# Kernel optimization log

Hardware: AMD Instinct MI355X
Metric: run time of the kernel (lower is better)

The kernel has to match this reference:

```python
import jax, jax.numpy as jnp
import numpy as np

B, L, C, H = 8, 1024, 512, 8
D = C // H  # head_size = 64


def setup_inputs() -> dict:
    key = jax.random.key(0)
    k1, k2, k3, k4, k5, k6 = jax.random.split(key, 6)
    x = jax.random.normal(k1, (B, L, C), dtype=jnp.float32)
    adj = jax.random.randint(k2, (B, L, L), 0, 2).astype(jnp.float32)
    distance = jax.random.randint(k3, (B, L, L), 0, 3).astype(jnp.float32)
    # nn.Linear(dim, 3*dim, bias=False): stored as y = x @ W; init ~ U(-1/sqrt(C), 1/sqrt(C))
    bound = 1.0 / np.sqrt(C)
    w_qkv = jax.random.uniform(k4, (C, 3 * C), minval=-bound, maxval=bound, dtype=jnp.float32)
    w_proj = jax.random.uniform(k5, (C, C), minval=-bound, maxval=bound, dtype=jnp.float32)
    # struct_gamma is zero-init in the module; use small random values so biases are exercised
    gamma = 0.1 * jax.random.normal(k6, (H, 5), dtype=jnp.float32)
    return {"x": x, "adj": adj, "distance": distance,
            "w_qkv": w_qkv, "w_proj": w_proj, "gamma": gamma}


def reference(x, adj, distance, w_qkv, w_proj, gamma):
    b, l, c = x.shape
    scale = jnp.asarray(np.sqrt(D), x.dtype)
    qkv = x @ w_qkv                                    # [B,L,3C]
    q, k, v = jnp.split(qkv, 3, axis=-1)
    q = q.reshape(b, l, H, D).transpose(0, 2, 1, 3)     # [B,H,L,D]
    k = k.reshape(b, l, H, D).transpose(0, 2, 1, 3)
    v = v.reshape(b, l, H, D).transpose(0, 2, 1, 3)
    s = jnp.einsum('bhid,bhjd->bhij', q, k) / scale     # [B,H,L,L]

    # has_cls=True: zero row 0 and col 0 of adj
    adj_local = adj.at[:, 0, :].set(0.0).at[:, :, 0].set(0.0)
    adj_t = adj_local.transpose(0, 2, 1)
    b_fwd = adj_local                                   # direct edges
    b_bwd = adj_t
    b_dist_fwd = (distance > 0).astype(x.dtype)         # multi-hop reachability
    b_dist_bwd = (distance.transpose(0, 2, 1) > 0).astype(x.dtype)
    b_struct = (jnp.einsum('bik,bjk->bij', adj_local, adj_local) > 0).astype(x.dtype)

    biases = jnp.stack([b_fwd, b_bwd, b_dist_fwd, b_dist_bwd, b_struct], axis=1)  # [B,5,L,L]
    s = s + jnp.einsum('hk,bkij->bhij', gamma, biases)

    attn = jax.nn.softmax(s, axis=-1)
    out = jnp.einsum('bhij,bhjd->bhid', attn, v)        # [B,H,L,D]
    out = out.transpose(0, 2, 1, 3).reshape(b, l, c)
    return out @ w_proj
```

## Files before the change

kernel.cpp:

```cpp
#include <hip/hip_runtime.h>
#include <hip/hip_bf16.h>
#include <stdint.h>

#define NB 8
#define NL 1024
#define NC 512
#define NH 8
#define ND 64

typedef __attribute__((ext_vector_type(8))) short short8;
typedef __attribute__((ext_vector_type(4))) float f32x4;
typedef unsigned long long u64;

__device__ __forceinline__ short f2bf(float f) {
  union { float f; uint32_t u; } v; v.f = f;
  uint32_t r = v.u + 0x7FFFu + ((v.u >> 16) & 1u);
  return (short)(r >> 16);
}

#define MFMA16(a, b, c) __builtin_amdgcn_mfma_f32_16x16x32_bf16((a), (b), (c), 0, 0, 0)

__global__ __launch_bounds__(256) void pack_k(const float* __restrict__ adj,
                                              const float* __restrict__ dist,
                                              u64* __restrict__ padj,
                                              u64* __restrict__ pdist) {
  int row = blockIdx.x;
  int i = row & (NL - 1);
  int wv = threadIdx.x >> 6, lane = threadIdx.x & 63;
  const float* asrc = adj + (size_t)row * NL;
  const float* dsrc = dist + (size_t)row * NL;
  #pragma unroll
  for (int it = 0; it < 4; it++) {
    int j = wv * 256 + it * 64 + lane;
    float a = asrc[j];
    float d = dsrc[j];
    u64 am = __ballot((a != 0.0f) && (i != 0) && (j != 0));
    u64 dm = __ballot(d > 0.0f);
    if (lane == 0) {
      padj[(size_t)row * 16 + wv * 4 + it] = am;
      pdist[(size_t)row * 16 + wv * 4 + it] = dm;
    }
  }
}

__global__ __launch_bounds__(256) void bits_k(const u64* __restrict__ padj,
                                              const u64* __restrict__ pdist,
                                              unsigned char* __restrict__ bits) {
  __shared__ u64 Pi[64][17], Pj[64][17];
  __shared__ u64 DiW[64], DjW[64];
  int b = blockIdx.z, i0 = blockIdx.y * 64, j0 = blockIdx.x * 64;
  int t = threadIdx.x;
  int jw = j0 >> 6, iw = i0 >> 6;
  const u64* pa = padj + (size_t)b * NL * 16;
  const u64* pd = pdist + (size_t)b * NL * 16;
  #pragma unroll
  for (int s = 0; s < 4; s++) {
    int idx = s * 256 + t; int r = idx >> 4, w = idx & 15;
    Pi[r][w] = pa[(size_t)(i0 + r) * 16 + w];
    Pj[r][w] = pa[(size_t)(j0 + r) * 16 + w];
  }
  if (t < 64) DiW[t] = pd[(size_t)(i0 + t) * 16 + jw];
  else if (t < 128) DjW[t - 64] = pd[(size_t)(j0 + t - 64) * 16 + iw];
  __syncthreads();
  const size_t base = (size_t)b * NL * NL;
  int jj0 = (t & 15) * 4;
  #pragma unroll
  for (int s = 0; s < 4; s++) {
    int ii = (t >> 4) + s * 16;
    u64 fwdw = Pi[ii][jw];
    u64 dfw = DiW[ii];
    uint32_t acc = 0;
    #pragma unroll
    for (int q = 0; q < 4; q++) {
      int jj = jj0 + q;
      unsigned v = 0;
      v |= (unsigned)((fwdw >> jj) & 1);
      v |= (unsigned)((Pj[jj][iw] >> ii) & 1) << 1;
      v |= (unsigned)((dfw >> jj) & 1) << 2;
      v |= (unsigned)((DjW[jj] >> ii) & 1) << 3;
      #pragma unroll 1
      for (int w = 0; w < 16; w++) {
        if (Pi[ii][w] & Pj[jj][w]) { v |= 16; break; }
      }
      acc |= v << (8 * q);
    }
    *(uint32_t*)&bits[base + (size_t)(i0 + ii) * NL + j0 + jj0] = acc;
  }
}

__global__ __launch_bounds__(256) void qkv_gemm_k(const float* __restrict__ x,
                                                  const float* __restrict__ w,
                                                  unsigned short* __restrict__ qb,
                                                  unsigned short* __restrict__ kb,
                                                  unsigned short* __restrict__ vb) {
  __shared__ short Al[64][40];
  __shared__ short Bl[64][40];
  int t = threadIdx.x;
  int wv = t >> 6, lane = t & 63, lg = lane >> 4, lm = lane & 15;
  int wr = wv >> 1, wc = wv & 1;
  int M0 = blockIdx.y * 64, N0 = blockIdx.x * 64;
  f32x4 zero4 = {0.f, 0.f, 0.f, 0.f};
  f32x4 acc[2][2] = {{zero4, zero4}, {zero4, zero4}};
  for (int k0 = 0; k0 < NC; k0 += 32) {
    {
      int row = t >> 2, cc = (t & 3) * 8;
      const float* src = x + (size_t)(M0 + row) * NC + k0 + cc;
      float4 v0 = *(const float4*)src;
      float4 v1 = *(const float4*)(src + 4);
      short8 s8;
      s8[0] = f2bf(v0.x); s8[1] = f2bf(v0.y); s8[2] = f2bf(v0.z); s8[3] = f2bf(v0.w);
      s8[4] = f2bf(v1.x); s8[5] = f2bf(v1.y); s8[6] = f2bf(v1.z); s8[7] = f2bf(v1.w);
      *(short8*)&Al[row][cc] = s8;
    }
    {
      int kk = t >> 3, cc = (t & 7) * 8;
      const float* src = w + (size_t)(k0 + kk) * (3 * NC) + N0 + cc;
      float4 v0 = *(const float4*)src;
      float4 v1 = *(const float4*)(src + 4);
      Bl[cc + 0][kk] = f2bf(v0.x); Bl[cc + 1][kk] = f2bf(v0.y);
      Bl[cc + 2][kk] = f2bf(v0.z); Bl[cc + 3][kk] = f2bf(v0.w);
      Bl[cc + 4][kk] = f2bf(v1.x); Bl[cc + 5][kk] = f2bf(v1.y);
      Bl[cc + 6][kk] = f2bf(v1.z); Bl[cc + 7][kk] = f2bf(v1.w);
    }
    __syncthreads();
    short8 af[2], bfr[2];
    af[0] = *(short8*)&Al[wr * 32 + lm][lg * 8];
    af[1] = *(short8*)&Al[wr * 32 + 16 + lm][lg * 8];
    bfr[0] = *(short8*)&Bl[wc * 32 + lm][lg * 8];
    bfr[1] = *(short8*)&Bl[wc * 32 + 16 + lm][lg * 8];
    #pragma unroll
    for (int mi = 0; mi < 2; mi++)
      #pragma unroll
      for (int ni = 0; ni < 2; ni++)
        acc[mi][ni] = MFMA16(af[mi], bfr[ni], acc[mi][ni]);
    __syncthreads();
  }
  #pragma unroll
  for (int mi = 0; mi < 2; mi++)
    #pragma unroll
    for (int ni = 0; ni < 2; ni++)
      #pragma unroll
      for (int r = 0; r < 4; r++) {
        int m = M0 + wr * 32 + mi * 16 + lg * 4 + r;
        int n = N0 + wc * 32 + ni * 16 + lm;
        int which = n >> 9, c = n & 511;
        int h = c >> 6, d = c & 63;
        int bb = m >> 10, ll = m & 1023;
        unsigned short* dst = which == 0 ? qb : (which == 1 ? kb : vb);
        dst[(((size_t)bb * NH + h) * NL + ll) * ND + d] = (unsigned short)f2bf(acc[mi][ni][r]);
      }
}

__global__ __launch_bounds__(256) void attn_k(const unsigned short* __restrict__ qb,
                                              const unsigned short* __restrict__ kb,
                                              const unsigned short* __restrict__ vb,
                                              const unsigned char* __restrict__ bits,
                                              const float* __restrict__ gamma,
                                              unsigned short* __restrict__ ao) {
  __shared__ short Kl[64][72];
  __shared__ short Vt[64][72];
  __shared__ short Pl[64][72];
  __shared__ float lut[32];
  int b = blockIdx.z, h = blockIdx.y, q0 = blockIdx.x * 64;
  int t = threadIdx.x, wv = t >> 6, lane = t & 63, lg = lane >> 4, lm = lane & 15;
  if (t < 32) {
    float s = 0.f;
    #pragma unroll
    for (int k = 0; k < 5; k++) if ((t >> k) & 1) s += gamma[h * 5 + k];
    lut[t] = s;
  }
  const size_t bh = ((size_t)b * NH + h) * NL;
  short8 qf[2];
  {
    const unsigned short* src = qb + (bh + q0 + wv * 16 + lm) * ND + lg * 8;
    qf[0] = *(const short8*)src;
    qf[1] = *(const short8*)(src + 32);
  }
  f32x4 zero4 = {0.f, 0.f, 0.f, 0.f};
  f32x4 oacc[4] = {zero4, zero4, zero4, zero4};
  float m_run[4], l_run[4];
  #pragma unroll
  for (int r = 0; r < 4; r++) { m_run[r] = -1e30f; l_run[r] = 0.f; }
  __syncthreads();
  for (int j0 = 0; j0 < NL; j0 += 64) {
    {
      int r = t >> 2, cc = (t & 3) * 16;
      const unsigned short* ks = kb + (bh + j0 + r) * ND + cc;
      *(short8*)&Kl[r][cc]     = *(const short8*)ks;
      *(short8*)&Kl[r][cc + 8] = *(const short8*)(ks + 8);
      const unsigned short* vs = vb + (bh + j0 + r) * ND + cc;
      short8 v0 = *(const short8*)vs;
      short8 v1 = *(const short8*)(vs + 8);
      #pragma unroll
      for (int jj = 0; jj < 8; jj++) Vt[cc + jj][r] = v0[jj];
      #pragma unroll
      for (int jj = 0; jj < 8; jj++) Vt[cc + 8 + jj][r] = v1[jj];
    }
    __syncthreads();
    f32x4 sf[4];
    #pragma unroll
    for (int ni = 0; ni < 4; ni++) {
      short8 b0 = *(short8*)&Kl[ni * 16 + lm][lg * 8];
      short8 b1 = *(short8*)&Kl[ni * 16 + lm][32 + lg * 8];
      f32x4 c = {0.f, 0.f, 0.f, 0.f};
      c = MFMA16(qf[0], b0, c);
      c = MFMA16(qf[1], b1, c);
      sf[ni] = c;
    }
    float svv[4][4];
    #pragma unroll
    for (int ni = 0; ni < 4; ni++)
      #pragma unroll
      for (int r = 0; r < 4; r++) {
        int qi = q0 + wv * 16 + lg * 4 + r;
        int kj = j0 + ni * 16 + lm;
        unsigned char bt = bits[((size_t)b * NL + qi) * NL + kj];
        svv[ni][r] = sf[ni][r] * 0.125f + lut[bt & 31];
      }
    float nm[4], fac[4], rsum[4];
    #pragma unroll
    for (int r = 0; r < 4; r++) {
      float mx = fmaxf(fmaxf(svv[0][r], svv[1][r]), fmaxf(svv[2][r], svv[3][r]));
      mx = fmaxf(mx, __shfl_xor(mx, 1));
      mx = fmaxf(mx, __shfl_xor(mx, 2));
      mx = fmaxf(mx, __shfl_xor(mx, 4));
      mx = fmaxf(mx, __shfl_xor(mx, 8));
      nm[r] = fmaxf(m_run[r], mx);
      fac[r] = __expf(m_run[r] - nm[r]);
      m_run[r] = nm[r];
      rsum[r] = 0.f;
    }
    #pragma unroll
    for (int ni = 0; ni < 4; ni++)
      #pragma unroll
      for (int r = 0; r < 4; r++) {
        float p = __expf(svv[ni][r] - nm[r]);
        svv[ni][r] = p;
        rsum[r] += p;
      }
    #pragma unroll
    for (int r = 0; r < 4; r++) {
      rsum[r] += __shfl_xor(rsum[r], 1);
      rsum[r] += __shfl_xor(rsum[r], 2);
      rsum[r] += __shfl_xor(rsum[r], 4);
      rsum[r] += __shfl_xor(rsum[r], 8);
      l_run[r] = l_run[r] * fac[r] + rsum[r];
    }
    #pragma unroll
    for (int ni = 0; ni < 4; ni++)
      #pragma unroll
      for (int r = 0; r < 4; r++)
        Pl[wv * 16 + lg * 4 + r][ni * 16 + lm] = f2bf(svv[ni][r]);
    #pragma unroll
    for (int di = 0; di < 4; di++)
      #pragma unroll
      for (int r = 0; r < 4; r++)
        oacc[di][r] *= fac[r];
    short8 pa0 = *(short8*)&Pl[wv * 16 + lm][lg * 8];
    short8 pa1 = *(short8*)&Pl[wv * 16 + lm][32 + lg * 8];
    #pragma unroll
    for (int di = 0; di < 4; di++) {
      short8 vb0 = *(short8*)&Vt[di * 16 + lm][lg * 8];
      short8 vb1 = *(short8*)&Vt[di * 16 + lm][32 + lg * 8];
      oacc[di] = MFMA16(pa0, vb0, oacc[di]);
      oacc[di] = MFMA16(pa1, vb1, oacc[di]);
    }
    __syncthreads();
  }
  #pragma unroll
  for (int di = 0; di < 4; di++)
    #pragma unroll
    for (int r = 0; r < 4; r++) {
      int qi = q0 + wv * 16 + lg * 4 + r;
      int d = di * 16 + lm;
      ao[((size_t)b * NL + qi) * NC + h * ND + d] =
          (unsigned short)f2bf(oacc[di][r] / l_run[r]);
    }
}

__global__ __launch_bounds__(256) void proj_gemm_k(const unsigned short* __restrict__ ao,
                                                   const float* __restrict__ w,
                                                   float* __restrict__ out) {
  __shared__ short Al[64][40];
  __shared__ short Bl[64][40];
  int t = threadIdx.x;
  int wv = t >> 6, lane = t & 63, lg = lane >> 4, lm = lane & 15;
  int wr = wv >> 1, wc = wv & 1;
  int M0 = blockIdx.y * 64, N0 = blockIdx.x * 64;
  f32x4 zero4 = {0.f, 0.f, 0.f, 0.f};
  f32x4 acc[2][2] = {{zero4, zero4}, {zero4, zero4}};
  for (int k0 = 0; k0 < NC; k0 += 32) {
    {
      int row = t >> 2, cc = (t & 3) * 8;
      *(short8*)&Al[row][cc] = *(const short8*)(ao + (size_t)(M0 + row) * NC + k0 + cc);
    }
    {
      int kk = t >> 3, cc = (t & 7) * 8;
      const float* src = w + (size_t)(k0 + kk) * NC + N0 + cc;
      float4 v0 = *(const float4*)src;
      float4 v1 = *(const float4*)(src + 4);
      Bl[cc + 0][kk] = f2bf(v0.x); Bl[cc + 1][kk] = f2bf(v0.y);
      Bl[cc + 2][kk] = f2bf(v0.z); Bl[cc + 3][kk] = f2bf(v0.w);
      Bl[cc + 4][kk] = f2bf(v1.x); Bl[cc + 5][kk] = f2bf(v1.y);
      Bl[cc + 6][kk] = f2bf(v1.z); Bl[cc + 7][kk] = f2bf(v1.w);
    }
    __syncthreads();
    short8 af[2], bfr[2];
    af[0] = *(short8*)&Al[wr * 32 + lm][lg * 8];
    af[1] = *(short8*)&Al[wr * 32 + 16 + lm][lg * 8];
    bfr[0] = *(short8*)&Bl[wc * 32 + lm][lg * 8];
    bfr[1] = *(short8*)&Bl[wc * 32 + 16 + lm][lg * 8];
    #pragma unroll
    for (int mi = 0; mi < 2; mi++)
      #pragma unroll
      for (int ni = 0; ni < 2; ni++)
        acc[mi][ni] = MFMA16(af[mi], bfr[ni], acc[mi][ni]);
    __syncthreads();
  }
  #pragma unroll
  for (int mi = 0; mi < 2; mi++)
    #pragma unroll
    for (int ni = 0; ni < 2; ni++)
      #pragma unroll
      for (int r = 0; r < 4; r++) {
        int m = M0 + wr * 32 + mi * 16 + lg * 4 + r;
        int n = N0 + wc * 32 + ni * 16 + lm;
        out[(size_t)m * NC + n] = acc[mi][ni][r];
      }
}

extern "C" void kernel_launch(void* const* d_in, const int* in_sizes, int n_in,
                              void* d_out, int out_size, void* d_ws, size_t ws_size,
                              hipStream_t stream) {
  (void)in_sizes; (void)n_in; (void)out_size; (void)ws_size;
  const float* x      = (const float*)d_in[0];
  const float* adj    = (const float*)d_in[1];
  const float* dist   = (const float*)d_in[2];
  const float* w_qkv  = (const float*)d_in[3];
  const float* w_proj = (const float*)d_in[4];
  const float* gamma  = (const float*)d_in[5];
  float* out = (float*)d_out;

  char* ws = (char*)d_ws;
  size_t off = 0;
  auto take = [&](size_t bytes) -> char* {
    char* p = ws + off;
    off += (bytes + 255) & ~(size_t)255;
    return p;
  };
  unsigned short* qb = (unsigned short*)take((size_t)NB * NH * NL * ND * 2);
  unsigned short* kb = (unsigned short*)take((size_t)NB * NH * NL * ND * 2);
  unsigned short* vb = (unsigned short*)take((size_t)NB * NH * NL * ND * 2);
  u64* padj  = (u64*)take((size_t)NB * NL * 16 * 8);
  u64* pdist = (u64*)take((size_t)NB * NL * 16 * 8);
  unsigned char* bits = (unsigned char*)take((size_t)NB * NL * NL);
  unsigned short* ao = (unsigned short*)take((size_t)NB * NL * NC * 2);

  pack_k<<<dim3(NB * NL), dim3(256), 0, stream>>>(adj, dist, padj, pdist);
  qkv_gemm_k<<<dim3(24, 128), dim3(256), 0, stream>>>(x, w_qkv, qb, kb, vb);
  bits_k<<<dim3(16, 16, NB), dim3(256), 0, stream>>>(padj, pdist, bits);
  attn_k<<<dim3(16, NH, NB), dim3(256), 0, stream>>>(qb, kb, vb, bits, gamma, ao);
  proj_gemm_k<<<dim3(8, 128), dim3(256), 0, stream>>>(ao, w_proj, out);
}
```

Before: 320.6 us.

## Pre-transpose V and read K/V fragments directly from global memory in attention

Adds a separate kernel that transposes V into a [D, L] layout per head. The attention kernel then loads K and V^T MFMA fragments straight from global memory instead of staging them through shared memory. This removes the LDS tiles, the scalar transpose scatter and both per-iteration barriers. The 1/sqrt(D) scale is also folded into Q when it is written in the QKV GEMM. In exchange, each wave reads K/V independently from global/L2, which adds redundant traffic, and there is one more kernel launch plus an extra V-sized buffer.

```diff
diff --git a/kernel.cpp b/kernel.cpp
--- a/kernel.cpp
+++ b/kernel.cpp
@@ -146,20 +146,44 @@
         int which = n >> 9, c = n & 511;
         int h = c >> 6, d = c & 63;
         int bb = m >> 10, ll = m & 1023;
-        unsigned short* dst = which == 0 ? qb : (which == 1 ? kb : vb);
-        dst[(((size_t)bb * NH + h) * NL + ll) * ND + d] = (unsigned short)f2bf(acc[mi][ni][r]);
-      }
+        float val = acc[mi][ni][r];
+        unsigned short* dst;
+        if (which == 0) { dst = qb; val *= 0.125f; }
+        else dst = (which == 1) ? kb : vb;
+        dst[(((size_t)bb * NH + h) * NL + ll) * ND + d] = (unsigned short)f2bf(val);
+      }
+}
+
+__global__ __launch_bounds__(256) void vt_k(const unsigned short* __restrict__ vb,
+                                            unsigned short* __restrict__ vtb) {
+  __shared__ short T[64][68];
+  int b = blockIdx.z, h = blockIdx.y, l0 = blockIdx.x * 64;
+  int t = threadIdx.x;
+  const size_t bh = (size_t)b * NH + h;
+  {
+    int r = t >> 2, c0 = (t & 3) * 16;
+    const unsigned short* src = vb + ((bh * NL) + l0 + r) * ND + c0;
+    *(short8*)&T[r][c0]     = *(const short8*)src;
+    *(short8*)&T[r][c0 + 8] = *(const short8*)(src + 8);
+  }
+  __syncthreads();
+  #pragma unroll
+  for (int it = 0; it < 2; it++) {
+    int d = (t >> 3) + it * 32, lc = (t & 7) * 8;
+    short8 v;
+    #pragma unroll
+    for (int j = 0; j < 8; j++) v[j] = T[lc + j][d];
+    *(short8*)(vtb + (bh * ND + d) * NL + l0 + lc) = v;
+  }
 }
 
 __global__ __launch_bounds__(256) void attn_k(const unsigned short* __restrict__ qb,
                                               const unsigned short* __restrict__ kb,
-                                              const unsigned short* __restrict__ vb,
+                                              const unsigned short* __restrict__ vtb,
                                               const unsigned char* __restrict__ bits,
                                               const float* __restrict__ gamma,
                                               unsigned short* __restrict__ ao) {
-  __shared__ short Kl[64][72];
-  __shared__ short Vt[64][72];
-  __shared__ short Pl[64][72];
+  __shared__ short Pl[64][68];
   __shared__ float lut[32];
   int b = blockIdx.z, h = blockIdx.y, q0 = blockIdx.x * 64;
   int t = threadIdx.x, wv = t >> 6, lane = t & 63, lg = lane >> 4, lm = lane & 15;
@@ -170,6 +194,8 @@
     lut[t] = s;
   }
   const size_t bh = ((size_t)b * NH + h) * NL;
+  const unsigned short* Kbase = kb + bh * ND;
+  const unsigned short* Vbase = vtb + bh * ND;
   short8 qf[2];
   {
     const unsigned short* src = qb + (bh + q0 + wv * 16 + lm) * ND + lg * 8;
@@ -183,25 +209,12 @@
   for (int r = 0; r < 4; r++) { m_run[r] = -1e30f; l_run[r] = 0.f; }
   __syncthreads();
   for (int j0 = 0; j0 < NL; j0 += 64) {
-    {
-      int r = t >> 2, cc = (t & 3) * 16;
-      const unsigned short* ks = kb + (bh + j0 + r) * ND + cc;
-      *(short8*)&Kl[r][cc]     = *(const short8*)ks;
-      *(short8*)&Kl[r][cc + 8] = *(const short8*)(ks + 8);
-      const unsigned short* vs = vb + (bh + j0 + r) * ND + cc;
-      short8 v0 = *(const short8*)vs;
-      short8 v1 = *(const short8*)(vs + 8);
-      #pragma unroll
-      for (int jj = 0; jj < 8; jj++) Vt[cc + jj][r] = v0[jj];
-      #pragma unroll
-      for (int jj = 0; jj < 8; jj++) Vt[cc + 8 + jj][r] = v1[jj];
-    }
-    __syncthreads();
     f32x4 sf[4];
     #pragma unroll
     for (int ni = 0; ni < 4; ni++) {
-      short8 b0 = *(short8*)&Kl[ni * 16 + lm][lg * 8];
-      short8 b1 = *(short8*)&Kl[ni * 16 + lm][32 + lg * 8];
+      const unsigned short* kp = Kbase + (size_t)(j0 + ni * 16 + lm) * ND + lg * 8;
+      short8 b0 = *(const short8*)kp;
+      short8 b1 = *(const short8*)(kp + 32);
       f32x4 c = {0.f, 0.f, 0.f, 0.f};
       c = MFMA16(qf[0], b0, c);
       c = MFMA16(qf[1], b1, c);
@@ -215,7 +228,7 @@
         int qi = q0 + wv * 16 + lg * 4 + r;
         int kj = j0 + ni * 16 + lm;
         unsigned char bt = bits[((size_t)b * NL + qi) * NL + kj];
-        svv[ni][r] = sf[ni][r] * 0.125f + lut[bt & 31];
+        svv[ni][r] = sf[ni][r] + lut[bt & 31];
       }
     float nm[4], fac[4], rsum[4];
     #pragma unroll
@@ -260,12 +273,12 @@
     short8 pa1 = *(short8*)&Pl[wv * 16 + lm][32 + lg * 8];
     #pragma unroll
     for (int di = 0; di < 4; di++) {
-      short8 vb0 = *(short8*)&Vt[di * 16 + lm][lg * 8];
-      short8 vb1 = *(short8*)&Vt[di * 16 + lm][32 + lg * 8];
+      const unsigned short* vp = Vbase + (size_t)(di * 16 + lm) * NL + j0 + lg * 8;
+      short8 vb0 = *(const short8*)vp;
+      short8 vb1 = *(const short8*)(vp + 32);
       oacc[di] = MFMA16(pa0, vb0, oacc[di]);
       oacc[di] = MFMA16(pa1, vb1, oacc[di]);
     }
-    __syncthreads();
   }
   #pragma unroll
   for (int di = 0; di < 4; di++)
@@ -351,6 +364,7 @@
   unsigned short* qb = (unsigned short*)take((size_t)NB * NH * NL * ND * 2);
   unsigned short* kb = (unsigned short*)take((size_t)NB * NH * NL * ND * 2);
   unsigned short* vb = (unsigned short*)take((size_t)NB * NH * NL * ND * 2);
+  unsigned short* vtb = (unsigned short*)take((size_t)NB * NH * NL * ND * 2);
   u64* padj  = (u64*)take((size_t)NB * NL * 16 * 8);
   u64* pdist = (u64*)take((size_t)NB * NL * 16 * 8);
   unsigned char* bits = (unsigned char*)take((size_t)NB * NL * NL);
@@ -358,7 +372,8 @@
 
   pack_k<<<dim3(NB * NL), dim3(256), 0, stream>>>(adj, dist, padj, pdist);
   qkv_gemm_k<<<dim3(24, 128), dim3(256), 0, stream>>>(x, w_qkv, qb, kb, vb);
+  vt_k<<<dim3(16, NH, NB), dim3(256), 0, stream>>>(vb, vtb);
   bits_k<<<dim3(16, 16, NB), dim3(256), 0, stream>>>(padj, pdist, bits);
-  attn_k<<<dim3(16, NH, NB), dim3(256), 0, stream>>>(qb, kb, vb, bits, gamma, ao);
+  attn_k<<<dim3(16, NH, NB), dim3(256), 0, stream>>>(qb, kb, vtb, bits, gamma, ao);
   proj_gemm_k<<<dim3(8, 128), dim3(256), 0, stream>>>(ao, w_proj, out);
 }
```

After: 372.2 us. +16.1%, slower.
